# Performance work log

Hardware: AMD Instinct MI355X
Metric: run time of the kernel (lower is better)

The kernel has to match this reference:

```python
import jax, jax.numpy as jnp
import numpy as np

KS = 3          # deformable kernel size
N = KS * KS     # 9 sampling points
PAD = 1         # zero padding before sampling


def setup_inputs() -> dict:
    key = jax.random.key(0)
    k = jax.random.split(key, 4)
    b, c, h, w = 8, 64, 128, 128
    x = jax.random.normal(k[0], (b, c, h, w), jnp.float32)
    # offset-prediction conv: Conv2d(c, 2*N, 3, padding=1, stride=1) with bias
    w_off = jax.random.normal(k[1], (2 * N, c, 3, 3), jnp.float32) * 0.01
    b_off = jax.random.normal(k[2], (2 * N,), jnp.float32) * 0.01
    # main conv: Conv2d(c, c, 3, stride=3, bias=None) applied to rearranged samples
    w_conv = jax.random.normal(k[3], (c, c, KS, KS), jnp.float32) * (1.0 / np.sqrt(c * N))
    return {"x": x, "w_off": w_off, "b_off": b_off, "w_conv": w_conv}


def _deform_conv2d(x, w_off, b_off, w_conv):
    b, c, h, w = x.shape
    # 1) predict offsets: (b, 2N, h, w)
    offset = jax.lax.conv_general_dilated(
        x, w_off, (1, 1), ((PAD, PAD), (PAD, PAD)),
        dimension_numbers=("NCHW", "OIHW", "NCHW"))
    offset = offset + b_off[None, :, None, None]
    offset = offset.transpose(0, 2, 3, 1)  # (b, h, w, 2N), first N = rows, last N = cols

    # 2) sampling positions p = p_0 + p_n + offset (in zero-padded coords)
    dx, dy = jnp.meshgrid(
        jnp.arange(-(KS - 1) // 2, (KS - 1) // 2 + 1),
        jnp.arange(-(KS - 1) // 2, (KS - 1) // 2 + 1), indexing="ij")
    pn_x = dx.reshape(-1).astype(x.dtype)  # (N,)
    pn_y = dy.reshape(-1).astype(x.dtype)
    r0 = jnp.arange(1, h + 1, dtype=x.dtype)  # p_0 starts at 1 (padding shift)
    c0 = jnp.arange(1, w + 1, dtype=x.dtype)
    p_x = offset[..., :N] + pn_x + r0[None, :, None, None]   # (b,h,w,N)
    p_y = offset[..., N:] + pn_y + c0[None, None, :, None]

    xp = jnp.pad(x, ((0, 0), (0, 0), (PAD, PAD), (PAD, PAD)))
    Hp, Wp = h + 2 * PAD, w + 2 * PAD

    fx = jnp.floor(p_x)
    fy = jnp.floor(p_y)
    q_lt_x = jnp.clip(fx, 0, Hp - 1).astype(jnp.int32)
    q_lt_y = jnp.clip(fy, 0, Wp - 1).astype(jnp.int32)
    q_rb_x = jnp.clip(fx + 1, 0, Hp - 1).astype(jnp.int32)
    q_rb_y = jnp.clip(fy + 1, 0, Wp - 1).astype(jnp.int32)
    p_x = jnp.clip(p_x, 0, Hp - 1)
    p_y = jnp.clip(p_y, 0, Wp - 1)

    # bilinear weights (b,h,w,N); q values are non-differentiable (int)
    g_lt = (1 + (q_lt_x - p_x)) * (1 + (q_lt_y - p_y))
    g_rb = (1 - (q_rb_x - p_x)) * (1 - (q_rb_y - p_y))
    g_lb = (1 + (q_lt_x - p_x)) * (1 - (q_rb_y - p_y))
    g_rt = (1 - (q_rb_x - p_x)) * (1 + (q_lt_y - p_y))

    xp_flat = xp.reshape(b, c, Hp * Wp)

    def gather(qx, qy):
        idx = (qx * Wp + qy).reshape(b, 1, h * w * N)
        out = jnp.take_along_axis(
            xp_flat, jnp.broadcast_to(idx, (b, c, h * w * N)), axis=2)
        return out.reshape(b, c, h, w, N)

    x_off = (g_lt[:, None] * gather(q_lt_x, q_lt_y)
             + g_rb[:, None] * gather(q_rb_x, q_rb_y)
             + g_lb[:, None] * gather(q_lt_x, q_rb_y)
             + g_rt[:, None] * gather(q_rb_x, q_lt_y))  # (b,c,h,w,N)

    # 3) final KSxKS conv with stride KS over the rearranged samples is exactly
    #    a contraction over the N sampling points (sample n = kernel tap (i,j), n=i*KS+j)
    out = jnp.einsum("bchwn,ocn->bohw", x_off, w_conv.reshape(c, c, N))
    return out


def reference(x, w_off, b_off, w_conv):
    return _deform_conv2d(x, w_off, b_off, w_conv) + x
```

## Files before the change

### kernel.cpp

```cpp
#include <hip/hip_runtime.h>


typedef _Float16 h2    __attribute__((ext_vector_type(2)));
typedef _Float16 f16x8 __attribute__((ext_vector_type(8)));
typedef float    f32x4 __attribute__((ext_vector_type(4)));

#define MFMAH(a, b, c) __builtin_amdgcn_mfma_f32_16x16x32_f16(a, b, c, 0, 0, 0)

#define RAW_SZ  68608
#define W_OFF   68608
#define W_SZ    73728
#define OFV_OFF 142336
#define SFB_OFF 148480
#define LDS_TOT 148496

__device__ __forceinline__ unsigned short f2h(float f) {
    return __builtin_bit_cast(unsigned short, (_Float16)f);
}
__device__ __forceinline__ float h2f_bits(unsigned u) {
    return (float)__builtin_bit_cast(_Float16, (unsigned short)(u & 0xffffu));
}
__device__ __forceinline__ unsigned dup16(float g) {
    _Float16 t = (_Float16)g;
    h2 r = {t, t};
    return __builtin_bit_cast(unsigned, r);
}

__device__ __forceinline__ void blend8(const uint4* clo, const uint4* chi, uint4 gq,
                                       f16x8& bfr0, f16x8& bfr1) {
    h2 g0 = __builtin_bit_cast(h2, gq.x), g1 = __builtin_bit_cast(h2, gq.y);
    h2 g2 = __builtin_bit_cast(h2, gq.z), g3 = __builtin_bit_cast(h2, gq.w);
    const unsigned* c0 = (const unsigned*)&clo[0];
    const unsigned* c1 = (const unsigned*)&clo[1];
    const unsigned* c2 = (const unsigned*)&clo[2];
    const unsigned* c3 = (const unsigned*)&clo[3];
    const unsigned* e0 = (const unsigned*)&chi[0];
    const unsigned* e1 = (const unsigned*)&chi[1];
    const unsigned* e2 = (const unsigned*)&chi[2];
    const unsigned* e3 = (const unsigned*)&chi[3];
    unsigned owl[4], owh[4];
#pragma unroll
    for (int d = 0; d < 4; ++d) {
        h2 sl = __builtin_bit_cast(h2, c0[d]) * g0;
        sl = __builtin_elementwise_fma(__builtin_bit_cast(h2, c1[d]), g1, sl);
        sl = __builtin_elementwise_fma(__builtin_bit_cast(h2, c2[d]), g2, sl);
        sl = __builtin_elementwise_fma(__builtin_bit_cast(h2, c3[d]), g3, sl);
        owl[d] = __builtin_bit_cast(unsigned, sl);
        h2 sh = __builtin_bit_cast(h2, e0[d]) * g0;
        sh = __builtin_elementwise_fma(__builtin_bit_cast(h2, e1[d]), g1, sh);
        sh = __builtin_elementwise_fma(__builtin_bit_cast(h2, e2[d]), g2, sh);
        sh = __builtin_elementwise_fma(__builtin_bit_cast(h2, e3[d]), g3, sh);
        owh[d] = __builtin_bit_cast(unsigned, sh);
    }
    bfr0 = __builtin_bit_cast(f16x8, *(const uint4*)owl);
    bfr1 = __builtin_bit_cast(f16x8, *(const uint4*)owh);
}

__global__ __launch_bounds__(256) void k_prep_xt(const float* __restrict__ x,
                                                 unsigned short* __restrict__ xt) {
    __shared__ float xs[64][129];
    const int bh = blockIdx.x;
    const int h = bh & 127, b = bh >> 7;
    const float* xr = x + ((size_t)b * 64 * 128 + h) * 128;
    for (int idx = threadIdx.x; idx < 8192; idx += 256) {
        int c = idx >> 7, w = idx & 127;
        xs[c][w] = xr[(size_t)c * 16384 + w];
    }
    __syncthreads();
    unsigned short* xto = xt + ((size_t)bh << 13);
    for (int j = threadIdx.x; j < 1024; j += 256) {
        int w = j >> 3, c0 = (j & 7) << 3;
        unsigned short tmp[8];
#pragma unroll
        for (int e = 0; e < 8; ++e) tmp[e] = f2h(xs[c0 + e][w]);
        *(uint4*)(xto + w * 64 + c0) = *(const uint4*)tmp;
    }
}

__global__ void k_prep_w(const float* __restrict__ w_conv, const float* __restrict__ w_off,
                         unsigned short* __restrict__ w_m2, unsigned short* __restrict__ woff2) {
    int t = blockIdx.x * 256 + threadIdx.x;
    if (t < 36864) {
        int r = t & 511;
        int fid = t >> 9;
        int l15 = r >> 5, q4 = (r >> 3) & 3, e = t & 7;
        int chunk = fid & 1, of = (fid >> 1) & 3, n = fid >> 3;
        int o = of * 16 + l15, c = chunk * 32 + q4 * 8 + e;
        w_m2[t] = f2h(w_conv[(o * 64 + c) * 9 + n]);
    }
    int t2 = t - 36864;
    if (t2 >= 0 && t2 < 18432) {
        int r = t2 & 511;
        int fid = t2 >> 9;
        int l15 = r >> 5, q4 = (r >> 3) & 3, e = t2 & 7;
        int kc = fid & 1, half = (fid >> 1) & 1, rj = fid >> 2;
        int k = half * 16 + l15, c = kc * 32 + q4 * 8 + e;
        woff2[t2] = (k < 18) ? f2h(w_off[(k * 64 + c) * 9 + rj]) : (unsigned short)0;
    }
}

__global__ __launch_bounds__(512, 2) void k_fused(
    const float* __restrict__ x, const unsigned short* __restrict__ xt,
    const unsigned short* __restrict__ w_m2g, const unsigned short* __restrict__ woff2g,
    const float* __restrict__ b_off, float* __restrict__ out) {

    extern __shared__ __align__(16) unsigned char lds[];
    unsigned char* raw  = lds;
    _Float16*      wlds = (_Float16*)(lds + W_OFF);
    _Float16*      offv = (_Float16*)(lds + OFV_OFF);
    int*           sfbp = (int*)(lds + SFB_OFF);

    const int wk = ((blockIdx.x & 7) << 7) | (blockIdx.x >> 3);
    const int b = wk >> 7, h = wk & 127;

    const int tid  = threadIdx.x;
    const int lane = tid & 63, wid = tid >> 6;
    const int l15  = lane & 15, q4 = lane >> 4;
    const int lofs = ((l15 << 2) + q4) << 3;
    const int px   = wid * 16 + l15;

    const unsigned short* xtb = xt + ((size_t)b << 20);

    if (tid == 0) *sfbp = 0;

    for (int idx = tid; idx < 4288; idx += 512) {
        int rec = idx >> 3, cc = idx & 7;
        int rl = rec / 134, col = rec - rl * 134;
        int xr = h - 2 + rl, xc = col - 3;
        uint4 v = make_uint4(0, 0, 0, 0);
        if (xr >= 0 && xr < 128 && xc >= 0 && xc < 128)
            v = *(const uint4*)(xtb + ((((size_t)xr << 7) + xc) << 6) + (cc << 3));
        int slot = (xr + 4) & 3;
        *(uint4*)(raw + ((slot * 134 + col) << 7) + ((cc ^ (col & 7)) << 4)) = v;
    }
    for (int idx = tid; idx < 2304; idx += 512)
        ((uint4*)wlds)[idx] = ((const uint4*)woff2g)[idx];
    __syncthreads();

    {
        f32x4 o0a = {0,0,0,0}, o0b = {0,0,0,0}, o1a = {0,0,0,0}, o1b = {0,0,0,0};
        f16x8 bfgA, af0A, af1A, bfgB, af0B, af1B;

#define ALOAD(s, S)                                                                      \
        {                                                                                \
            constexpr int rj = (s) >> 1, kc = (s) & 1;                                   \
            const int colw = px + (rj % 3) + 2;                                          \
            const int slt  = (h + (rj / 3) + 3) & 3;                                     \
            bfg##S = *(const f16x8*)(raw + ((slt * 134 + colw) << 7) + ((((kc << 2) + q4) ^ (colw & 7)) << 4)); \
            af0##S = *(const f16x8*)(wlds + ((((rj * 2 + 0) << 1) + kc) << 9) + lofs);   \
            af1##S = *(const f16x8*)(wlds + ((((rj * 2 + 1) << 1) + kc) << 9) + lofs);   \
        }
#define AEXEC(S, P)                                                                      \
        {                                                                                \
            o0##P = MFMAH(af0##S, bfg##S, o0##P);                                        \
            o1##P = MFMAH(af1##S, bfg##S, o1##P);                                        \
        }
        ALOAD(0, A)
        ALOAD(1, B)  AEXEC(A, a)
        ALOAD(2, A)  AEXEC(B, b)
        ALOAD(3, B)  AEXEC(A, a)
        ALOAD(4, A)  AEXEC(B, b)
        ALOAD(5, B)  AEXEC(A, a)
        ALOAD(6, A)  AEXEC(B, b)
        ALOAD(7, B)  AEXEC(A, a)
        ALOAD(8, A)  AEXEC(B, b)
        ALOAD(9, B)  AEXEC(A, a)
        ALOAD(10, A) AEXEC(B, b)
        ALOAD(11, B) AEXEC(A, a)
        ALOAD(12, A) AEXEC(B, b)
        ALOAD(13, B) AEXEC(A, a)
        ALOAD(14, A) AEXEC(B, b)
        ALOAD(15, B) AEXEC(A, a)
        ALOAD(16, A) AEXEC(B, b)
        ALOAD(17, B) AEXEC(A, a)
                     AEXEC(B, b)
#undef ALOAD
#undef AEXEC
        float4 bo = *(const float4*)(b_off + (q4 << 2));
        float2 bo2 = *(const float2*)(b_off + 16);
        const float bov[4] = {bo.x, bo.y, bo.z, bo.w};
#pragma unroll
        for (int rg = 0; rg < 4; ++rg) {
            int o = (q4 << 2) + rg;
            offv[px * 24 + o] = (_Float16)(o0a[rg] + o0b[rg] + bov[rg]);
            if (q4 == 0 && rg < 2)
                offv[px * 24 + 16 + rg] = (_Float16)(o1a[rg] + o1b[rg] + (rg ? bo2.y : bo2.x));
        }
    }
    __syncthreads();

    for (int idx = tid; idx < 4608; idx += 512)
        ((uint4*)wlds)[idx] = ((const uint4*)w_m2g)[idx];
    for (int idx = tid; idx < 1152; idx += 512) {
        int n = idx % 9, p = idx / 9;
        int g = n / 3;
        float ox = (float)offv[p * 24 + n];
        float pxf = (float)(h + g) + ox;
        float fx = floorf(pxf);
        int t0 = (int)fminf(fmaxf(fx, 0.f), 129.f) + 1 - h - g;
        int t1 = (int)fminf(fmaxf(fx + 1.f, 0.f), 129.f) + 1 - h - g;
        if (((unsigned)t0 > 3u) | ((unsigned)t1 > 3u)) *sfbp = 1;
    }
    const size_t obase = ((size_t)b << 20) + h * 128 + px;
    float xres[4][4];
#pragma unroll
    for (int of = 0; of < 4; ++of)
#pragma unroll
        for (int rg = 0; rg < 4; ++rg)
            xres[of][rg] = x[obase + (size_t)((of << 4) + (q4 << 2) + rg) * 16384];
    __syncthreads();
    const bool slow = (*sfbp != 0);

    f32x4 acc[4];
#pragma unroll
    for (int of = 0; of < 4; ++of) acc[of] = (f32x4){0.f, 0.f, 0.f, 0.f};

    if (!slow) {
        const unsigned* op = (const unsigned*)(offv + px * 24);
        uint4 oA = *(const uint4*)op;
        uint4 oB = *(const uint4*)(op + 4);
        unsigned oC = op[8];
        const unsigned owr[9] = {oA.x, oA.y, oA.z, oA.w, oB.x, oB.y, oB.z, oB.w, oC};
#define OXQ(n) h2f_bits(owr[(n) >> 1] >> (((n) & 1) << 4))
#define OYQ(n) h2f_bits(owr[(9 + (n)) >> 1] >> (((9 + (n)) & 1) << 4))

        uint4 cloA[4], chiA[4], cloB[4], chiB[4];
        uint4 gqA, gqB;
        f16x8 waA[8], waB[8];
        uint4 pf[3];
        int prec[3], pcc[3];

#define PREF(ROW)                                                                        \
        {                                                                                \
            _Pragma("unroll")                                                            \
            for (int k = 0; k < 3; ++k) {                                                \
                int idx = tid + (k << 9);                                                \
                bool v = idx < 1072;                                                     \
                int rec = idx >> 3;                                                      \
                pcc[k] = idx & 7;                                                        \
                int xc = rec - 3;                                                        \
                uint4 vv = make_uint4(0, 0, 0, 0);                                       \
                if (v && (ROW) < 128 && xc >= 0 && xc < 128)                             \
                    vv = *(const uint4*)(xtb + ((((size_t)(ROW) << 7) + xc) << 6) + (pcc[k] << 3)); \
                prec[k] = v ? rec : -1;                                                  \
                pf[k] = vv;                                                              \
            }                                                                            \
        }
#define WRB(ROW)                                                                         \
        {                                                                                \
            const int slt = ((ROW) + 4) & 3;                                             \
            _Pragma("unroll")                                                            \
            for (int k = 0; k < 3; ++k)                                                  \
                if (prec[k] >= 0)                                                        \
                    *(uint4*)(raw + ((slt * 134 + prec[k]) << 7) + ((pcc[k] ^ (prec[k] & 7)) << 4)) = pf[k]; \
        }

#define TAPLOAD(n, S)                                                                    \
        {                                                                                \
            constexpr int g = (n) / 3, dj = (n) % 3;                                     \
            float ox = OXQ(n), oy = OYQ(n);                                              \
            float pxf = (float)(h + g) + ox, pyf = (float)(px + dj) + oy;                \
            float fx = floorf(pxf), fy = floorf(pyf);                                    \
            float qx0f = fminf(fmaxf(fx, 0.f), 129.f);                                   \
            float qx1f = fminf(fmaxf(fx + 1.f, 0.f), 129.f);                             \
            float qy0f = fminf(fmaxf(fy, 0.f), 129.f);                                   \
            float qy1f = fminf(fmaxf(fy + 1.f, 0.f), 129.f);                             \
            float pxc = fminf(fmaxf(pxf, 0.f), 129.f);                                   \
            float pyc = fminf(fmaxf(pyf, 0.f), 129.f);                                   \
            float ax0 = 1.f + (qx0f - pxc), ax1 = 1.f - (qx1f - pxc);                    \
            float ay0 = 1.f + (qy0f - pyc), ay1 = 1.f - (qy1f - pyc);                    \
            int r0 = (((int)qx0f + 3) & 3) * 134, r1 = (((int)qx1f + 3) & 3) * 134;      \
            int c0 = (int)qy0f + 2, c1 = (int)qy1f + 2;                                  \
            int blt = (r0 + c0) << 7, brb = (r1 + c1) << 7;                              \
            int blb = (r0 + c1) << 7, brt = (r1 + c0) << 7;                              \
            int z0 = ((q4 ^ c0) & 7) << 4, z1 = ((q4 ^ c1) & 7) << 4;                    \
            clo##S[0] = *(const uint4*)(raw + blt + z0);                                 \
            chi##S[0] = *(const uint4*)(raw + blt + (z0 ^ 64));                          \
            clo##S[1] = *(const uint4*)(raw + brb + z1);                                 \
            chi##S[1] = *(const uint4*)(raw + brb + (z1 ^ 64));                          \
            clo##S[2] = *(const uint4*)(raw + blb + z1);                                 \
            chi##S[2] = *(const uint4*)(raw + blb + (z1 ^ 64));                          \
            clo##S[3] = *(const uint4*)(raw + brt + z0);                                 \
            chi##S[3] = *(const uint4*)(raw + brt + (z0 ^ 64));                          \
            gq##S = make_uint4(dup16(ax0 * ay0), dup16(ax1 * ay1),                       \
                               dup16(ax0 * ay1), dup16(ax1 * ay0));                      \
            _Pragma("unroll")                                                            \
            for (int of = 0; of < 4; ++of) {                                             \
                wa##S[2 * of]     = *(const f16x8*)(wlds + (((n) * 8 + of * 2 + 0) << 9) + lofs); \
                wa##S[2 * of + 1] = *(const f16x8*)(wlds + (((n) * 8 + of * 2 + 1) << 9) + lofs); \
            }                                                                            \
        }
#define TAPEXEC(S)                                                                       \
        {                                                                                \
            f16x8 bfr0, bfr1;                                                            \
            blend8(clo##S, chi##S, gq##S, bfr0, bfr1);                                   \
            _Pragma("unroll")                                                            \
            for (int of = 0; of < 4; ++of) {                                             \
                acc[of] = MFMAH(wa##S[2 * of],     bfr0, acc[of]);                       \
                acc[of] = MFMAH(wa##S[2 * of + 1], bfr1, acc[of]);                       \
            }                                                                            \
        }

        PREF(h + 2)
        TAPLOAD(0, A)
        TAPLOAD(1, B) TAPEXEC(A)
        TAPLOAD(2, A) TAPEXEC(B)
                      TAPEXEC(A)
        __syncthreads();
        WRB(h + 2)
        __syncthreads();
        PREF(h + 3)
        TAPLOAD(3, A)
        TAPLOAD(4, B) TAPEXEC(A)
        TAPLOAD(5, A) TAPEXEC(B)
                      TAPEXEC(A)
        __syncthreads();
        WRB(h + 3)
        __syncthreads();
        TAPLOAD(6, A)
        TAPLOAD(7, B) TAPEXEC(A)
        TAPLOAD(8, A) TAPEXEC(B)
                      TAPEXEC(A)
#undef TAPLOAD
#undef TAPEXEC
#undef PREF
#undef WRB
#undef OXQ
#undef OYQ
    } else {
        for (int n = 0; n < 9; ++n) {
            const int g = n / 3, dj = n % 3;
            float ox = (float)offv[px * 24 + n], oy = (float)offv[px * 24 + 9 + n];
            float pxf = (float)(h + g) + ox, pyf = (float)(px + dj) + oy;
            float fx = floorf(pxf), fy = floorf(pyf);
            float qx0f = fminf(fmaxf(fx, 0.f), 129.f);
            float qx1f = fminf(fmaxf(fx + 1.f, 0.f), 129.f);
            float qy0f = fminf(fmaxf(fy, 0.f), 129.f);
            float qy1f = fminf(fmaxf(fy + 1.f, 0.f), 129.f);
            float pxc = fminf(fmaxf(pxf, 0.f), 129.f);
            float pyc = fminf(fmaxf(pyf, 0.f), 129.f);
            float ax0 = 1.f + (qx0f - pxc), ax1 = 1.f - (qx1f - pxc);
            float ay0 = 1.f + (qy0f - pyc), ay1 = 1.f - (qy1f - pyc);
            int qx[2] = {(int)qx0f, (int)qx1f};
            int qy[2] = {(int)qy0f, (int)qy1f};
            uint4 clo[4], chi[4];
            const int rsel[4] = {0, 1, 0, 1}, csel[4] = {0, 1, 1, 0};
#pragma unroll
            for (int j = 0; j < 4; ++j) {
                int rx = qx[rsel[j]], ry = qy[csel[j]];
                bool v = (rx >= 1) & (rx <= 128) & (ry >= 1) & (ry <= 128);
                clo[j] = make_uint4(0, 0, 0, 0);
                chi[j] = make_uint4(0, 0, 0, 0);
                if (v) {
                    const unsigned short* gp = xtb + ((((size_t)(rx - 1) << 7) + (ry - 1)) << 6);
                    clo[j] = *(const uint4*)(gp + (q4 << 3));
                    chi[j] = *(const uint4*)(gp + (q4 << 3) + 32);
                }
            }
            uint4 gq = make_uint4(dup16(ax0 * ay0), dup16(ax1 * ay1),
                                  dup16(ax0 * ay1), dup16(ax1 * ay0));
            f16x8 bfr0, bfr1;
            blend8(clo, chi, gq, bfr0, bfr1);
#pragma unroll
            for (int of = 0; of < 4; ++of) {
                f16x8 a0 = *(const f16x8*)(wlds + ((n * 8 + of * 2 + 0) << 9) + lofs);
                f16x8 a1 = *(const f16x8*)(wlds + ((n * 8 + of * 2 + 1) << 9) + lofs);
                acc[of] = MFMAH(a0, bfr0, acc[of]);
                acc[of] = MFMAH(a1, bfr1, acc[of]);
            }
        }
    }

#pragma unroll
    for (int of = 0; of < 4; ++of)
#pragma unroll
        for (int rg = 0; rg < 4; ++rg)
            out[obase + (size_t)((of << 4) + (q4 << 2) + rg) * 16384] = acc[of][rg] + xres[of][rg];
}

extern "C" void kernel_launch(void* const* d_in, const int* in_sizes, int n_in,
                              void* d_out, int out_size, void* d_ws, size_t ws_size,
                              hipStream_t stream) {
    const float* x      = (const float*)d_in[0];
    const float* w_off  = (const float*)d_in[1];
    const float* b_off  = (const float*)d_in[2];
    const float* w_conv = (const float*)d_in[3];

    unsigned short* xt    = (unsigned short*)d_ws;
    unsigned short* w_m2  = xt + (size_t)8 * 128 * 128 * 64;
    unsigned short* woff2 = w_m2 + 9 * 64 * 64;

    hipFuncSetAttribute((const void*)k_fused,
                        hipFuncAttributeMaxDynamicSharedMemorySize, LDS_TOT);

    hipLaunchKernelGGL(k_prep_xt, dim3(1024), dim3(256), 0, stream, x, xt);
    hipLaunchKernelGGL(k_prep_w,  dim3(216),  dim3(256), 0, stream, w_conv, w_off, w_m2, woff2);
    hipLaunchKernelGGL(k_fused,   dim3(1024), dim3(512), LDS_TOT, stream,
                       x, xt, w_m2, woff2, b_off, (float*)d_out);
}
```

Before: 79.38 us.

## Split offset conv into separate kernel and process four rows per fused block

Moves the offset-prediction convolution out of the fused kernel into a new k_off kernel that writes fp16 offsets to global memory and sets a per-4-row fallback flag with atomics. The fused kernel now handles four output rows per block (256 blocks, one per CU), reusing the LDS-resident weight tile and the row ring buffer across rows so weights are loaded once per four rows. The cost is an extra launch, a global round-trip for the offsets, and lower occupancy (launch bounds 512,1 with 256 blocks), which may leave the machine underfilled.

New measurement: 163.8 us, median of 6. +106.4%, slower.

```diff
diff --git a/kernel.cpp b/kernel.cpp
--- a/kernel.cpp
+++ b/kernel.cpp
@@ -7,12 +7,8 @@
 
 #define MFMAH(a, b, c) __builtin_amdgcn_mfma_f32_16x16x32_f16(a, b, c, 0, 0, 0)
 
-#define RAW_SZ  68608
-#define W_OFF   68608
-#define W_SZ    73728
-#define OFV_OFF 142336
-#define SFB_OFF 148480
-#define LDS_TOT 148496
+#define RING_SZ 68608
+#define LDS_TOT (RING_SZ + 73728)
 
 __device__ __forceinline__ unsigned short f2h(float f) {
     return __builtin_bit_cast(unsigned short, (_Float16)f);
@@ -78,8 +74,10 @@
 }
 
 __global__ void k_prep_w(const float* __restrict__ w_conv, const float* __restrict__ w_off,
-                         unsigned short* __restrict__ w_m2, unsigned short* __restrict__ woff2) {
+                         unsigned short* __restrict__ w_m2, unsigned short* __restrict__ woff2,
+                         int* __restrict__ flags) {
     int t = blockIdx.x * 256 + threadIdx.x;
+    if (blockIdx.x == 0) flags[threadIdx.x] = 0;
     if (t < 36864) {
         int r = t & 511;
         int fid = t >> 9;
@@ -99,19 +97,14 @@
     }
 }
 
-__global__ __launch_bounds__(512, 2) void k_fused(
-    const float* __restrict__ x, const unsigned short* __restrict__ xt,
-    const unsigned short* __restrict__ w_m2g, const unsigned short* __restrict__ woff2g,
-    const float* __restrict__ b_off, float* __restrict__ out) {
-
-    extern __shared__ __align__(16) unsigned char lds[];
-    unsigned char* raw  = lds;
-    _Float16*      wlds = (_Float16*)(lds + W_OFF);
-    _Float16*      offv = (_Float16*)(lds + OFV_OFF);
-    int*           sfbp = (int*)(lds + SFB_OFF);
-
-    const int wk = ((blockIdx.x & 7) << 7) | (blockIdx.x >> 3);
-    const int b = wk >> 7, h = wk & 127;
+__global__ __launch_bounds__(256) void k_off(
+    const unsigned short* __restrict__ xt, const unsigned short* __restrict__ woff2,
+    const float* __restrict__ b_off, _Float16* __restrict__ offg,
+    int* __restrict__ flags) {
+    __shared__ __align__(16) unsigned char raw3[3 * 66 * 128];
+
+    const int gb = blockIdx.x;
+    const int wt = (gb & 1) << 6, h = (gb >> 1) & 127, b = gb >> 8;
 
     const int tid  = threadIdx.x;
     const int lane = tid & 63, wid = tid >> 6;
@@ -121,7 +114,81 @@
 
     const unsigned short* xtb = xt + ((size_t)b << 20);
 
-    if (tid == 0) *sfbp = 0;
+    for (int idx = tid; idx < 1584; idx += 256) {
+        int rec = idx >> 3, cc = idx & 7;
+        int rl = rec / 66, col = rec - rl * 66;
+        int xr = h - 1 + rl, xc = wt - 1 + col;
+        uint4 v = make_uint4(0, 0, 0, 0);
+        if (xr >= 0 && xr < 128 && xc >= 0 && xc < 128)
+            v = *(const uint4*)(xtb + ((((size_t)xr << 7) + xc) << 6) + (cc << 3));
+        *(uint4*)(raw3 + (rec << 7) + ((cc ^ (col & 7)) << 4)) = v;
+    }
+    __syncthreads();
+
+    f32x4 o0 = {0.f, 0.f, 0.f, 0.f}, o1 = {0.f, 0.f, 0.f, 0.f};
+#pragma unroll
+    for (int rj = 0; rj < 9; ++rj) {
+        const int dr = rj / 3, dj = rj % 3;
+        const int colw = px + dj;
+        const int recb = dr * 66 + colw;
+        const int swz  = colw & 7;
+#pragma unroll
+        for (int kc = 0; kc < 2; ++kc) {
+            f16x8 bfrag = *(const f16x8*)(raw3 + (recb << 7) + ((((kc << 2) + q4) ^ swz) << 4));
+            f16x8 a0 = *(const f16x8*)((const _Float16*)woff2 + ((((rj * 2 + 0) << 1) + kc) << 9) + lofs);
+            f16x8 a1 = *(const f16x8*)((const _Float16*)woff2 + ((((rj * 2 + 1) << 1) + kc) << 9) + lofs);
+            o0 = MFMAH(a0, bfrag, o0);
+            o1 = MFMAH(a1, bfrag, o1);
+        }
+    }
+
+    float4 bo = *(const float4*)(b_off + (q4 << 2));
+    float2 bo2 = *(const float2*)(b_off + 16);
+    const float bov[4] = {bo.x, bo.y, bo.z, bo.w};
+    const size_t pix = ((size_t)(b * 128 + h)) * 128 + wt + px;
+    _Float16* og = offg + pix * 24;
+
+    bool oow = false;
+#pragma unroll
+    for (int rg = 0; rg < 4; ++rg) {
+        int o = (q4 << 2) + rg;
+        _Float16 v16 = (_Float16)(o0[rg] + bov[rg]);
+        og[o] = v16;
+        if (o < 9) {
+            int g = o / 3;
+            float pxf = (float)(h + g) + (float)v16;
+            float fx = floorf(pxf);
+            int qx0 = (int)fminf(fmaxf(fx, 0.f), 129.f);
+            int qx1 = (int)fminf(fmaxf(fx + 1.f, 0.f), 129.f);
+            int t0 = qx0 - h - g + 1, t1 = qx1 - h - g + 1;
+            oow |= ((unsigned)t0 > 3u) | ((unsigned)t1 > 3u);
+        }
+        if (q4 == 0 && rg < 2)
+            og[16 + rg] = (_Float16)(o1[rg] + (rg ? bo2.y : bo2.x));
+    }
+    if (__any(oow) && lane == 0) atomicOr(flags + ((b << 5) | (h >> 2)), 1);
+}
+
+__global__ __launch_bounds__(512, 1) void k_fused(
+    const float* __restrict__ x, const unsigned short* __restrict__ xt,
+    const unsigned short* __restrict__ w_m2g, const _Float16* __restrict__ offg,
+    const int* __restrict__ flags, float* __restrict__ out) {
+
+    extern __shared__ __align__(16) unsigned char lds[];
+    unsigned char* raw  = lds;
+    _Float16*      wlds = (_Float16*)(lds + RING_SZ);
+
+    const int wk = ((blockIdx.x & 7) << 5) | (blockIdx.x >> 3);
+    const int b = wk >> 5, h4 = wk & 31, h = h4 << 2;
+
+    const int tid  = threadIdx.x;
+    const int lane = tid & 63, wid = tid >> 6;
+    const int l15  = lane & 15, q4 = lane >> 4;
+    const int lofs = ((l15 << 2) + q4) << 3;
+    const int px   = wid * 16 + l15;
+
+    const unsigned short* xtb = xt + ((size_t)b << 20);
+    const bool slow = (flags[(b << 5) | h4] != 0);
 
     for (int idx = tid; idx < 4288; idx += 512) {
         int rec = idx >> 3, cc = idx & 7;
@@ -130,252 +197,202 @@
         uint4 v = make_uint4(0, 0, 0, 0);
         if (xr >= 0 && xr < 128 && xc >= 0 && xc < 128)
             v = *(const uint4*)(xtb + ((((size_t)xr << 7) + xc) << 6) + (cc << 3));
-        int slot = (xr + 4) & 3;
-        *(uint4*)(raw + ((slot * 134 + col) << 7) + ((cc ^ (col & 7)) << 4)) = v;
-    }
-    for (int idx = tid; idx < 2304; idx += 512)
-        ((uint4*)wlds)[idx] = ((const uint4*)woff2g)[idx];
-    __syncthreads();
-
-    {
-        f32x4 o0a = {0,0,0,0}, o0b = {0,0,0,0}, o1a = {0,0,0,0}, o1b = {0,0,0,0};
-        f16x8 bfgA, af0A, af1A, bfgB, af0B, af1B;
-
-#define ALOAD(s, S)                                                                      \
-        {                                                                                \
-            constexpr int rj = (s) >> 1, kc = (s) & 1;                                   \
-            const int colw = px + (rj % 3) + 2;                                          \
-            const int slt  = (h + (rj / 3) + 3) & 3;                                     \
-            bfg##S = *(const f16x8*)(raw + ((slt * 134 + colw) << 7) + ((((kc << 2) + q4) ^ (colw & 7)) << 4)); \
-            af0##S = *(const f16x8*)(wlds + ((((rj * 2 + 0) << 1) + kc) << 9) + lofs);   \
-            af1##S = *(const f16x8*)(wlds + ((((rj * 2 + 1) << 1) + kc) << 9) + lofs);   \
-        }
-#define AEXEC(S, P)                                                                      \
-        {                                                                                \
-            o0##P = MFMAH(af0##S, bfg##S, o0##P);                                        \
-            o1##P = MFMAH(af1##S, bfg##S, o1##P);                                        \
-        }
-        ALOAD(0, A)
-        ALOAD(1, B)  AEXEC(A, a)
-        ALOAD(2, A)  AEXEC(B, b)
-        ALOAD(3, B)  AEXEC(A, a)
-        ALOAD(4, A)  AEXEC(B, b)
-        ALOAD(5, B)  AEXEC(A, a)
-        ALOAD(6, A)  AEXEC(B, b)
-        ALOAD(7, B)  AEXEC(A, a)
-        ALOAD(8, A)  AEXEC(B, b)
-        ALOAD(9, B)  AEXEC(A, a)
-        ALOAD(10, A) AEXEC(B, b)
-        ALOAD(11, B) AEXEC(A, a)
-        ALOAD(12, A) AEXEC(B, b)
-        ALOAD(13, B) AEXEC(A, a)
-        ALOAD(14, A) AEXEC(B, b)
-        ALOAD(15, B) AEXEC(A, a)
-        ALOAD(16, A) AEXEC(B, b)
-        ALOAD(17, B) AEXEC(A, a)
-                     AEXEC(B, b)
-#undef ALOAD
-#undef AEXEC
-        float4 bo = *(const float4*)(b_off + (q4 << 2));
-        float2 bo2 = *(const float2*)(b_off + 16);
-        const float bov[4] = {bo.x, bo.y, bo.z, bo.w};
-#pragma unroll
-        for (int rg = 0; rg < 4; ++rg) {
-            int o = (q4 << 2) + rg;
-            offv[px * 24 + o] = (_Float16)(o0a[rg] + o0b[rg] + bov[rg]);
-            if (q4 == 0 && rg < 2)
-                offv[px * 24 + 16 + rg] = (_Float16)(o1a[rg] + o1b[rg] + (rg ? bo2.y : bo2.x));
-        }
-    }
-    __syncthreads();
-
+        *(uint4*)(raw + (((xr + 4) & 3) * 134 + col << 7) + ((cc ^ (col & 7)) << 4)) = v;
+    }
     for (int idx = tid; idx < 4608; idx += 512)
         ((uint4*)wlds)[idx] = ((const uint4*)w_m2g)[idx];
-    for (int idx = tid; idx < 1152; idx += 512) {
-        int n = idx % 9, p = idx / 9;
-        int g = n / 3;
-        float ox = (float)offv[p * 24 + n];
-        float pxf = (float)(h + g) + ox;
-        float fx = floorf(pxf);
-        int t0 = (int)fminf(fmaxf(fx, 0.f), 129.f) + 1 - h - g;
-        int t1 = (int)fminf(fmaxf(fx + 1.f, 0.f), 129.f) + 1 - h - g;
-        if (((unsigned)t0 > 3u) | ((unsigned)t1 > 3u)) *sfbp = 1;
-    }
-    const size_t obase = ((size_t)b << 20) + h * 128 + px;
-    float xres[4][4];
-#pragma unroll
-    for (int of = 0; of < 4; ++of)
-#pragma unroll
-        for (int rg = 0; rg < 4; ++rg)
-            xres[of][rg] = x[obase + (size_t)((of << 4) + (q4 << 2) + rg) * 16384];
     __syncthreads();
-    const bool slow = (*sfbp != 0);
-
-    f32x4 acc[4];
-#pragma unroll
-    for (int of = 0; of < 4; ++of) acc[of] = (f32x4){0.f, 0.f, 0.f, 0.f};
+
+    uint4 pf[3];
+    int prec[3], pcc[3];
+    auto PREF = [&](int u) {
+#pragma unroll
+        for (int k = 0; k < 3; ++k) {
+            int idx = tid + (k << 9);
+            bool v = idx < 1072;
+            int rec = idx >> 3;
+            pcc[k] = idx & 7;
+            int xc = rec - 3;
+            uint4 vv = make_uint4(0, 0, 0, 0);
+            if (v && u >= 0 && u < 128 && xc >= 0 && xc < 128)
+                vv = *(const uint4*)(xtb + ((((size_t)u << 7) + xc) << 6) + (pcc[k] << 3));
+            prec[k] = v ? rec : -1;
+            pf[k] = vv;
+        }
+    };
+    auto WRB = [&](int u) {
+        const int slt = (u + 4) & 3;
+#pragma unroll
+        for (int k = 0; k < 3; ++k)
+            if (prec[k] >= 0)
+                *(uint4*)(raw + ((slt * 134 + prec[k]) << 7) + ((pcc[k] ^ (prec[k] & 7)) << 4)) = pf[k];
+    };
 
     if (!slow) {
-        const unsigned* op = (const unsigned*)(offv + px * 24);
-        uint4 oA = *(const uint4*)op;
-        uint4 oB = *(const uint4*)(op + 4);
-        unsigned oC = op[8];
-        const unsigned owr[9] = {oA.x, oA.y, oA.z, oA.w, oB.x, oB.y, oB.z, oB.w, oC};
-#define OXQ(n) h2f_bits(owr[(n) >> 1] >> (((n) & 1) << 4))
-#define OYQ(n) h2f_bits(owr[(9 + (n)) >> 1] >> (((9 + (n)) & 1) << 4))
-
         uint4 cloA[4], chiA[4], cloB[4], chiB[4];
         uint4 gqA, gqB;
         f16x8 waA[8], waB[8];
-        uint4 pf[3];
-        int prec[3], pcc[3];
-
-#define PREF(ROW)                                                                        \
-        {                                                                                \
-            _Pragma("unroll")                                                            \
-            for (int k = 0; k < 3; ++k) {                                                \
-                int idx = tid + (k << 9);                                                \
-                bool v = idx < 1072;                                                     \
-                int rec = idx >> 3;                                                      \
-                pcc[k] = idx & 7;                                                        \
-                int xc = rec - 3;                                                        \
-                uint4 vv = make_uint4(0, 0, 0, 0);                                       \
-                if (v && (ROW) < 128 && xc >= 0 && xc < 128)                             \
-                    vv = *(const uint4*)(xtb + ((((size_t)(ROW) << 7) + xc) << 6) + (pcc[k] << 3)); \
-                prec[k] = v ? rec : -1;                                                  \
-                pf[k] = vv;                                                              \
-            }                                                                            \
-        }
-#define WRB(ROW)                                                                         \
-        {                                                                                \
-            const int slt = ((ROW) + 4) & 3;                                             \
-            _Pragma("unroll")                                                            \
-            for (int k = 0; k < 3; ++k)                                                  \
-                if (prec[k] >= 0)                                                        \
-                    *(uint4*)(raw + ((slt * 134 + prec[k]) << 7) + ((pcc[k] ^ (prec[k] & 7)) << 4)) = pf[k]; \
-        }
+
+        for (int r = 0; r < 4; ++r) {
+            const int R = h + r;
+            const float rbF = (float)R;
+
+            const _Float16* obp = offg + ((size_t)((b * 128 + R)) * 128 + px) * 24;
+            uint4 oA = *(const uint4*)obp;
+            uint4 oB = *(const uint4*)(obp + 8);
+            unsigned oC = *(const unsigned*)(obp + 16);
+            const unsigned owr[9] = {oA.x, oA.y, oA.z, oA.w, oB.x, oB.y, oB.z, oB.w, oC};
+#define OXQ(n) h2f_bits(owr[(n) >> 1] >> (((n) & 1) << 4))
+#define OYQ(n) h2f_bits(owr[(9 + (n)) >> 1] >> (((9 + (n)) & 1) << 4))
+
+            const size_t obase = ((size_t)b << 20) + (size_t)R * 128 + px;
+            float xres[4][4];
+#pragma unroll
+            for (int of = 0; of < 4; ++of)
+#pragma unroll
+                for (int rg = 0; rg < 4; ++rg)
+                    xres[of][rg] = x[obase + (size_t)((of << 4) + (q4 << 2) + rg) * 16384];
+
+            f32x4 acc[4];
+#pragma unroll
+            for (int of = 0; of < 4; ++of) acc[of] = (f32x4){0.f, 0.f, 0.f, 0.f};
 
 #define TAPLOAD(n, S)                                                                    \
-        {                                                                                \
-            constexpr int g = (n) / 3, dj = (n) % 3;                                     \
-            float ox = OXQ(n), oy = OYQ(n);                                              \
-            float pxf = (float)(h + g) + ox, pyf = (float)(px + dj) + oy;                \
-            float fx = floorf(pxf), fy = floorf(pyf);                                    \
-            float qx0f = fminf(fmaxf(fx, 0.f), 129.f);                                   \
-            float qx1f = fminf(fmaxf(fx + 1.f, 0.f), 129.f);                             \
-            float qy0f = fminf(fmaxf(fy, 0.f), 129.f);                                   \
-            float qy1f = fminf(fmaxf(fy + 1.f, 0.f), 129.f);                             \
-            float pxc = fminf(fmaxf(pxf, 0.f), 129.f);                                   \
-            float pyc = fminf(fmaxf(pyf, 0.f), 129.f);                                   \
-            float ax0 = 1.f + (qx0f - pxc), ax1 = 1.f - (qx1f - pxc);                    \
-            float ay0 = 1.f + (qy0f - pyc), ay1 = 1.f - (qy1f - pyc);                    \
-            int r0 = (((int)qx0f + 3) & 3) * 134, r1 = (((int)qx1f + 3) & 3) * 134;      \
-            int c0 = (int)qy0f + 2, c1 = (int)qy1f + 2;                                  \
-            int blt = (r0 + c0) << 7, brb = (r1 + c1) << 7;                              \
-            int blb = (r0 + c1) << 7, brt = (r1 + c0) << 7;                              \
-            int z0 = ((q4 ^ c0) & 7) << 4, z1 = ((q4 ^ c1) & 7) << 4;                    \
-            clo##S[0] = *(const uint4*)(raw + blt + z0);                                 \
-            chi##S[0] = *(const uint4*)(raw + blt + (z0 ^ 64));                          \
-            clo##S[1] = *(const uint4*)(raw + brb + z1);                                 \
-            chi##S[1] = *(const uint4*)(raw + brb + (z1 ^ 64));                          \
-            clo##S[2] = *(const uint4*)(raw + blb + z1);                                 \
-            chi##S[2] = *(const uint4*)(raw + blb + (z1 ^ 64));                          \
-            clo##S[3] = *(const uint4*)(raw + brt + z0);                                 \
-            chi##S[3] = *(const uint4*)(raw + brt + (z0 ^ 64));                          \
-            gq##S = make_uint4(dup16(ax0 * ay0), dup16(ax1 * ay1),                       \
-                               dup16(ax0 * ay1), dup16(ax1 * ay0));                      \
-            _Pragma("unroll")                                                            \
-            for (int of = 0; of < 4; ++of) {                                             \
-                wa##S[2 * of]     = *(const f16x8*)(wlds + (((n) * 8 + of * 2 + 0) << 9) + lofs); \
-                wa##S[2 * of + 1] = *(const f16x8*)(wlds + (((n) * 8 + of * 2 + 1) << 9) + lofs); \
-            }                                                                            \
-        }
+            {                                                                            \
+                constexpr int g = (n) / 3, dj = (n) % 3;                                 \
+                float ox = OXQ(n), oy = OYQ(n);                                          \
+                float pxf = rbF + (float)g + ox, pyf = (float)(px + dj) + oy;            \
+                float fx = floorf(pxf), fy = floorf(pyf);                                \
+                float qx0f = fminf(fmaxf(fx, 0.f), 129.f);                               \
+                float qx1f = fminf(fmaxf(fx + 1.f, 0.f), 129.f);                         \
+                float qy0f = fminf(fmaxf(fy, 0.f), 129.f);                               \
+                float qy1f = fminf(fmaxf(fy + 1.f, 0.f), 129.f);                         \
+                float pxc = fminf(fmaxf(pxf, 0.f), 129.f);                               \
+                float pyc = fminf(fmaxf(pyf, 0.f), 129.f);                               \
+                float ax0 = 1.f + (qx0f - pxc), ax1 = 1.f - (qx1f - pxc);                \
+                float ay0 = 1.f + (qy0f - pyc), ay1 = 1.f - (qy1f - pyc);                \
+                int r0 = (((int)qx0f + 3) & 3) * 134, r1 = (((int)qx1f + 3) & 3) * 134;  \
+                int c0 = (int)qy0f + 2, c1 = (int)qy1f + 2;                              \
+                int blt = (r0 + c0) << 7, brb = (r1 + c1) << 7;                          \
+                int blb = (r0 + c1) << 7, brt = (r1 + c0) << 7;                          \
+                int z0 = ((q4 ^ c0) & 7) << 4, z1 = ((q4 ^ c1) & 7) << 4;                \
+                clo##S[0] = *(const uint4*)(raw + blt + z0);                             \
+                chi##S[0] = *(const uint4*)(raw + blt + (z0 ^ 64));                      \
+                clo##S[1] = *(const uint4*)(raw + brb + z1);                             \
+                chi##S[1] = *(const uint4*)(raw + brb + (z1 ^ 64));                      \
+                clo##S[2] = *(const uint4*)(raw + blb + z1);                             \
+                chi##S[2] = *(const uint4*)(raw + blb + (z1 ^ 64));                      \
+                clo##S[3] = *(const uint4*)(raw + brt + z0);                             \
+                chi##S[3] = *(const uint4*)(raw + brt + (z0 ^ 64));                      \
+                gq##S = make_uint4(dup16(ax0 * ay0), dup16(ax1 * ay1),                   \
+                                   dup16(ax0 * ay1), dup16(ax1 * ay0));                  \
+                _Pragma("unroll")                                                        \
+                for (int of = 0; of < 4; ++of) {                                         \
+                    wa##S[2 * of]     = *(const f16x8*)(wlds + (((n) * 8 + of * 2 + 0) << 9) + lofs); \
+                    wa##S[2 * of + 1] = *(const f16x8*)(wlds + (((n) * 8 + of * 2 + 1) << 9) + lofs); \
+                }                                                                        \
+            }
 #define TAPEXEC(S)                                                                       \
-        {                                                                                \
-            f16x8 bfr0, bfr1;                                                            \
-            blend8(clo##S, chi##S, gq##S, bfr0, bfr1);                                   \
-            _Pragma("unroll")                                                            \
-            for (int of = 0; of < 4; ++of) {                                             \
-                acc[of] = MFMAH(wa##S[2 * of],     bfr0, acc[of]);                       \
-                acc[of] = MFMAH(wa##S[2 * of + 1], bfr1, acc[of]);                       \
-            }                                                                            \
-        }
-
-        PREF(h + 2)
-        TAPLOAD(0, A)
-        TAPLOAD(1, B) TAPEXEC(A)
-        TAPLOAD(2, A) TAPEXEC(B)
-                      TAPEXEC(A)
-        __syncthreads();
-        WRB(h + 2)
-        __syncthreads();
-        PREF(h + 3)
-        TAPLOAD(3, A)
-        TAPLOAD(4, B) TAPEXEC(A)
-        TAPLOAD(5, A) TAPEXEC(B)
-                      TAPEXEC(A)
-        __syncthreads();
-        WRB(h + 3)
-        __syncthreads();
-        TAPLOAD(6, A)
-        TAPLOAD(7, B) TAPEXEC(A)
-        TAPLOAD(8, A) TAPEXEC(B)
-                      TAPEXEC(A)
+            {                                                                            \
+                f16x8 bfr0, bfr1;                                                        \
+                blend8(clo##S, chi##S, gq##S, bfr0, bfr1);                               \
+                _Pragma("unroll")                                                        \
+                for (int of = 0; of < 4; ++of) {                                         \
+                    acc[of] = MFMAH(wa##S[2 * of],     bfr0, acc[of]);                   \
+                    acc[of] = MFMAH(wa##S[2 * of + 1], bfr1, acc[of]);                   \
+                }                                                                        \
+            }
+
+            PREF(R + 2);
+            TAPLOAD(0, A)
+            TAPLOAD(1, B) TAPEXEC(A)
+            TAPLOAD(2, A) TAPEXEC(B)
+                          TAPEXEC(A)
+            __syncthreads(); WRB(R + 2); __syncthreads();
+
+            PREF(R + 3);
+            TAPLOAD(3, A)
+            TAPLOAD(4, B) TAPEXEC(A)
+            TAPLOAD(5, A) TAPEXEC(B)
+                          TAPEXEC(A)
+            __syncthreads(); WRB(R + 3); __syncthreads();
+
+            if (r < 3) PREF(R - 1);
+            TAPLOAD(6, A)
+            TAPLOAD(7, B) TAPEXEC(A)
+            TAPLOAD(8, A) TAPEXEC(B)
+                          TAPEXEC(A)
 #undef TAPLOAD
 #undef TAPEXEC
-#undef PREF
-#undef WRB
 #undef OXQ
 #undef OYQ
+
+#pragma unroll
+            for (int of = 0; of < 4; ++of)
+#pragma unroll
+                for (int rg = 0; rg < 4; ++rg)
+                    out[obase + (size_t)((of << 4) + (q4 << 2) + rg) * 16384] = acc[of][rg] + xres[of][rg];
+
+            if (r < 3) { __syncthreads(); WRB(R - 1); __syncthreads(); }
+        }
     } else {
-        for (int n = 0; n < 9; ++n) {
-            const int g = n / 3, dj = n % 3;
-            float ox = (float)offv[px * 24 + n], oy = (float)offv[px * 24 + 9 + n];
-            float pxf = (float)(h + g) + ox, pyf = (float)(px + dj) + oy;
-            float fx = floorf(pxf), fy = floorf(pyf);
-            float qx0f = fminf(fmaxf(fx, 0.f), 129.f);
-            float qx1f = fminf(fmaxf(fx + 1.f, 0.f), 129.f);
-            float qy0f = fminf(fmaxf(fy, 0.f), 129.f);
-            float qy1f = fminf(fmaxf(fy + 1.f, 0.f), 129.f);
-            float pxc = fminf(fmaxf(pxf, 0.f), 129.f);
-            float pyc = fminf(fmaxf(pyf, 0.f), 129.f);
-            float ax0 = 1.f + (qx0f - pxc), ax1 = 1.f - (qx1f - pxc);
-            float ay0 = 1.f + (qy0f - pyc), ay1 = 1.f - (qy1f - pyc);
-            int qx[2] = {(int)qx0f, (int)qx1f};
-            int qy[2] = {(int)qy0f, (int)qy1f};
-            uint4 clo[4], chi[4];
-            const int rsel[4] = {0, 1, 0, 1}, csel[4] = {0, 1, 1, 0};
-#pragma unroll
-            for (int j = 0; j < 4; ++j) {
-                int rx = qx[rsel[j]], ry = qy[csel[j]];
-                bool v = (rx >= 1) & (rx <= 128) & (ry >= 1) & (ry <= 128);
-                clo[j] = make_uint4(0, 0, 0, 0);
-                chi[j] = make_uint4(0, 0, 0, 0);
-                if (v) {
-                    const unsigned short* gp = xtb + ((((size_t)(rx - 1) << 7) + (ry - 1)) << 6);
-                    clo[j] = *(const uint4*)(gp + (q4 << 3));
-                    chi[j] = *(const uint4*)(gp + (q4 << 3) + 32);
+        for (int r = 0; r < 4; ++r) {
+            const int R = h + r;
+            const _Float16* obp = offg + ((size_t)((b * 128 + R)) * 128 + px) * 24;
+            const size_t obase = ((size_t)b << 20) + (size_t)R * 128 + px;
+            f32x4 acc[4];
+#pragma unroll
+            for (int of = 0; of < 4; ++of) acc[of] = (f32x4){0.f, 0.f, 0.f, 0.f};
+            for (int n = 0; n < 9; ++n) {
+                const int g = n / 3, dj = n % 3;
+                float ox = (float)obp[n], oy = (float)obp[9 + n];
+                float pxf = (float)(R + g) + ox, pyf = (float)(px + dj) + oy;
+                float fx = floorf(pxf), fy = floorf(pyf);
+                float qx0f = fminf(fmaxf(fx, 0.f), 129.f);
+                float qx1f = fminf(fmaxf(fx + 1.f, 0.f), 129.f);
+                float qy0f = fminf(fmaxf(fy, 0.f), 129.f);
+                float qy1f = fminf(fmaxf(fy + 1.f, 0.f), 129.f);
+                float pxc = fminf(fmaxf(pxf, 0.f), 129.f);
+                float pyc = fminf(fmaxf(pyf, 0.f), 129.f);
+                float ax0 = 1.f + (qx0f - pxc), ax1 = 1.f - (qx1f - pxc);
+                float ay0 = 1.f + (qy0f - pyc), ay1 = 1.f - (qy1f - pyc);
+                int qx[2] = {(int)qx0f, (int)qx1f};
+                int qy[2] = {(int)qy0f, (int)qy1f};
+                uint4 clo[4], chi[4];
+                const int rsel[4] = {0, 1, 0, 1}, csel[4] = {0, 1, 1, 0};
+#pragma unroll
+                for (int j = 0; j < 4; ++j) {
+                    int rx = qx[rsel[j]], ry = qy[csel[j]];
+                    bool v = (rx >= 1) & (rx <= 128) & (ry >= 1) & (ry <= 128);
+                    clo[j] = make_uint4(0, 0, 0, 0);
+                    chi[j] = make_uint4(0, 0, 0, 0);
+                    if (v) {
+                        const unsigned short* gp = xtb + ((((size_t)(rx - 1) << 7) + (ry - 1)) << 6);
+                        clo[j] = *(const uint4*)(gp + (q4 << 3));
+                        chi[j] = *(const uint4*)(gp + (q4 << 3) + 32);
+                    }
+                }
+                uint4 gq = make_uint4(dup16(ax0 * ay0), dup16(ax1 * ay1),
+                                      dup16(ax0 * ay1), dup16(ax1 * ay0));
+                f16x8 bfr0, bfr1;
+                blend8(clo, chi, gq, bfr0, bfr1);
+#pragma unroll
+                for (int of = 0; of < 4; ++of) {
+                    f16x8 a0 = *(const f16x8*)(wlds + ((n * 8 + of * 2 + 0) << 9) + lofs);
+                    f16x8 a1 = *(const f16x8*)(wlds + ((n * 8 + of * 2 + 1) << 9) + lofs);
+                    acc[of] = MFMAH(a0, bfr0, acc[of]);
+                    acc[of] = MFMAH(a1, bfr1, acc[of]);
                 }
             }
-            uint4 gq = make_uint4(dup16(ax0 * ay0), dup16(ax1 * ay1),
-                                  dup16(ax0 * ay1), dup16(ax1 * ay0));
-            f16x8 bfr0, bfr1;
-            blend8(clo, chi, gq, bfr0, bfr1);
-#pragma unroll
-            for (int of = 0; of < 4; ++of) {
-                f16x8 a0 = *(const f16x8*)(wlds + ((n * 8 + of * 2 + 0) << 9) + lofs);
-                f16x8 a1 = *(const f16x8*)(wlds + ((n * 8 + of * 2 + 1) << 9) + lofs);
-                acc[of] = MFMAH(a0, bfr0, acc[of]);
-                acc[of] = MFMAH(a1, bfr1, acc[of]);
-            }
+#pragma unroll
+            for (int of = 0; of < 4; ++of)
+#pragma unroll
+                for (int rg = 0; rg < 4; ++rg) {
+                    size_t a = obase + (size_t)((of << 4) + (q4 << 2) + rg) * 16384;
+                    out[a] = acc[of][rg] + x[a];
+                }
         }
     }
-
-#pragma unroll
-    for (int of = 0; of < 4; ++of)
-#pragma unroll
-        for (int rg = 0; rg < 4; ++rg)
-            out[obase + (size_t)((of << 4) + (q4 << 2) + rg) * 16384] = acc[of][rg] + xres[of][rg];
 }
 
 extern "C" void kernel_launch(void* const* d_in, const int* in_sizes, int n_in,
@@ -388,13 +405,17 @@
 
     unsigned short* xt    = (unsigned short*)d_ws;
     unsigned short* w_m2  = xt + (size_t)8 * 128 * 128 * 64;
-    unsigned short* woff2 = w_m2 + 9 * 64 * 64;
+    unsigned short* woff2 = w_m2 + 36864;
+    _Float16*       offg  = (_Float16*)(woff2 + 18432);
+    int*            flags = (int*)(offg + (size_t)131072 * 24);
 
     hipFuncSetAttribute((const void*)k_fused,
                         hipFuncAttributeMaxDynamicSharedMemorySize, LDS_TOT);
 
     hipLaunchKernelGGL(k_prep_xt, dim3(1024), dim3(256), 0, stream, x, xt);
-    hipLaunchKernelGGL(k_prep_w,  dim3(216),  dim3(256), 0, stream, w_conv, w_off, w_m2, woff2);
-    hipLaunchKernelGGL(k_fused,   dim3(1024), dim3(512), LDS_TOT, stream,
-                       x, xt, w_m2, woff2, b_off, (float*)d_out);
-}
+    hipLaunchKernelGGL(k_prep_w,  dim3(216),  dim3(256), 0, stream, w_conv, w_off, w_m2, woff2, flags);
+    hipLaunchKernelGGL(k_off,     dim3(2048), dim3(256), 0, stream,
+                       xt, woff2, b_off, offg, flags);
+    hipLaunchKernelGGL(k_fused,   dim3(256),  dim3(512), LDS_TOT, stream,
+                       x, xt, w_m2, offg, flags, (float*)d_out);
+}
```
